# Performance work log

Hardware: AMD Instinct MI355X
Metric: run time of the kernel (lower is better)

## Reference

```python
import jax, jax.numpy as jnp
import numpy as np

N_HEADS = 16


def setup_inputs() -> dict:
    key = jax.random.key(0)
    ks = jax.random.split(key, 5)
    B, S, D = 2, 2048, 1024
    x = jax.random.normal(ks[0], (B, S, D), dtype=jnp.float32)
    Wqkv = jax.random.normal(ks[1], (D, 3 * D), dtype=jnp.float32) * (1.0 / np.sqrt(D))
    bqkv = jax.random.normal(ks[2], (3 * D,), dtype=jnp.float32) * 0.02
    Wout = jax.random.normal(ks[3], (D, D), dtype=jnp.float32) * (1.0 / np.sqrt(D))
    bout = jax.random.normal(ks[4], (D,), dtype=jnp.float32) * 0.02
    return {"x": x, "Wqkv": Wqkv, "bqkv": bqkv, "Wout": Wout, "bout": bout}


def reference(x, Wqkv, bqkv, Wout, bout):
    B, S, D = x.shape
    H = N_HEADS
    dh = D // H
    # qkv projection, then view as [B,S,H,3*dh] and chunk on last dim
    # (matches torch: per-head q/k/v are interleaved slices of the projection)
    qkv = (x @ Wqkv + bqkv).reshape(B, S, H, 3 * dh).transpose(0, 2, 1, 3)  # [B,H,S,3dh]
    q, k, v = jnp.split(qkv, 3, axis=-1)  # each [B,H,S,dh]
    scale = jnp.asarray(1.0 / np.sqrt(dh), dtype=x.dtype)
    scores = jnp.einsum('bhqd,bhkd->bhqk', q, k) * scale  # [B,H,S,S]
    causal = jnp.tril(jnp.ones((S, S), dtype=bool))
    scores = jnp.where(causal, scores, jnp.asarray(-jnp.inf, dtype=scores.dtype))
    attn_w = jax.nn.softmax(scores, axis=-1)
    attn = jnp.einsum('bhqk,bhkd->bhqd', attn_w, v)  # [B,H,S,dh]
    attn = attn.transpose(0, 2, 1, 3).reshape(B, S, D)
    return attn @ Wout + bout
```

## Files before the change

### kernel.cpp

```cpp
#include <hip/hip_runtime.h>
#include <hip/hip_bf16.h>
#include <cstdint>
#include <cstddef>

typedef __hip_bfloat16 bf16;
typedef short bf16x4 __attribute__((ext_vector_type(4)));
typedef short bf16x8 __attribute__((ext_vector_type(8)));
typedef float f32x4 __attribute__((ext_vector_type(4)));

#define LOG2E 1.44269504088896f

static constexpr int Bb = 2, S = 2048, D = 1024, H = 16, DH = 64;

__device__ inline short f2bf_bits(float f) {
  bf16 b = __float2bfloat16(f);
  short s;
  __builtin_memcpy(&s, &b, 2);
  return s;
}
__device__ inline float bfbits2f(short s) {
  uint32_t u = ((uint32_t)(uint16_t)s) << 16;
  float f;
  __builtin_memcpy(&f, &u, 4);
  return f;
}

__global__ void transpose_cvt_k(const float* __restrict__ in, bf16* __restrict__ out,
                                int R, int C) {
  __shared__ float t[32][33];
  int c0 = blockIdx.x * 32, r0 = blockIdx.y * 32;
  int tx = threadIdx.x, ty = threadIdx.y;
#pragma unroll
  for (int i = 0; i < 4; i++) {
    int r = ty + i * 8;
    t[r][tx] = in[(size_t)(r0 + r) * C + c0 + tx];
  }
  __syncthreads();
#pragma unroll
  for (int i = 0; i < 4; i++) {
    int c = ty + i * 8;
    out[(size_t)(c0 + c) * R + r0 + tx] = __float2bfloat16(t[tx][c]);
  }
}

__global__ void cvt_f32_bf16_k(const float* __restrict__ in, bf16* __restrict__ out) {
  size_t i = ((size_t)blockIdx.x * 256 + threadIdx.x) * 8;
  f32x4 a = *(const f32x4*)(in + i);
  f32x4 b = *(const f32x4*)(in + i + 4);
  bf16x8 v;
#pragma unroll
  for (int j = 0; j < 4; j++) { v[j] = f2bf_bits(a[j]); v[4 + j] = f2bf_bits(b[j]); }
  *(bf16x8*)((short*)out + i) = v;
}

__global__ __launch_bounds__(256) void gemm_qkv(
    const bf16* __restrict__ A, const bf16* __restrict__ Bt,
    const float* __restrict__ bias,
    bf16* __restrict__ Qb, bf16* __restrict__ Kb, bf16* __restrict__ Vtb) {
  constexpr int K = 1024;
  __shared__ __align__(16) short smA[128 * 32];
  __shared__ __align__(16) short smB[128 * 32];

  const int tid = threadIdx.x;
  const int wave = tid >> 6, lane = tid & 63;
  const int quad = lane >> 4, l16 = lane & 15;
  const int m0 = blockIdx.y * 128, n0 = blockIdx.x * 128;
  const int wm = wave >> 1, wn = wave & 1;

  f32x4 acc[4][4];
#pragma unroll
  for (int i = 0; i < 4; i++)
#pragma unroll
    for (int j = 0; j < 4; j++) acc[i][j] = {0.f, 0.f, 0.f, 0.f};

  const int srow = lane >> 2;
  const int scol = (lane & 3) * 8;

  for (int k0 = 0; k0 < K; k0 += 32) {
#pragma unroll
    for (int half = 0; half < 2; half++) {
      int row = half * 64 + wave * 16 + srow;
      const bf16* ga = A + (size_t)(m0 + row) * K + k0 + scol;
      const bf16* gb = Bt + (size_t)(n0 + row) * K + k0 + scol;
      __builtin_amdgcn_global_load_lds(
          (const __attribute__((address_space(1))) void*)ga,
          (__attribute__((address_space(3))) void*)&smA[(half * 64 + wave * 16) * 32],
          16, 0, 0);
      __builtin_amdgcn_global_load_lds(
          (const __attribute__((address_space(1))) void*)gb,
          (__attribute__((address_space(3))) void*)&smB[(half * 64 + wave * 16) * 32],
          16, 0, 0);
    }
    __syncthreads();

    bf16x8 af[4], bf_[4];
#pragma unroll
    for (int mi = 0; mi < 4; mi++)
      af[mi] = *(const bf16x8*)&smA[(wm * 64 + mi * 16 + l16) * 32 + quad * 8];
#pragma unroll
    for (int ni = 0; ni < 4; ni++)
      bf_[ni] = *(const bf16x8*)&smB[(wn * 64 + ni * 16 + l16) * 32 + quad * 8];
#pragma unroll
    for (int mi = 0; mi < 4; mi++)
#pragma unroll
      for (int ni = 0; ni < 4; ni++)
        acc[mi][ni] = __builtin_amdgcn_mfma_f32_16x16x32_bf16(
            af[mi], bf_[ni], acc[mi][ni], 0, 0, 0);
    __syncthreads();
  }

#pragma unroll
  for (int ni = 0; ni < 4; ni++) {
    const int cs = n0 + wn * 64 + ni * 16;
    const int h = cs / 192;
    const int roff = cs - h * 192;
    const float bv = bias[cs + l16];
#pragma unroll
    for (int mi = 0; mi < 4; mi++) {
      const int t0 = m0 + wm * 64 + mi * 16 + quad * 4;
      const int b = t0 >> 11, s0 = t0 & 2047;
      if (roff < 64) {
        const int dh = roff + l16;
        size_t base = ((size_t)(b * H + h) * S + s0) * 64 + dh;
#pragma unroll
        for (int r = 0; r < 4; r++)
          Qb[base + (size_t)r * 64] = __float2bfloat16(acc[mi][ni][r] + bv);
      } else if (roff < 128) {
        const int dh = roff - 64 + l16;
        size_t base = ((size_t)(b * H + h) * S + s0) * 64 + dh;
#pragma unroll
        for (int r = 0; r < 4; r++)
          Kb[base + (size_t)r * 64] = __float2bfloat16(acc[mi][ni][r] + bv);
      } else {
        const int dh = roff - 128 + l16;
        size_t base = ((size_t)(b * H + h) * 64 + dh) * S + s0;
        bf16x4 vv;
#pragma unroll
        for (int r = 0; r < 4; r++) vv[r] = f2bf_bits(acc[mi][ni][r] + bv);
        *(bf16x4*)((short*)Vtb + base) = vv;
      }
    }
  }
}

template <typename TC, int BN>
__global__ __launch_bounds__(256) void gemm_bt_bias(
    const bf16* __restrict__ A, const bf16* __restrict__ Bt,
    const float* __restrict__ bias, TC* __restrict__ C,
    int M, int N, int K) {
  constexpr int NF = BN / 32;
  __shared__ __align__(16) short smA[128 * 32];
  __shared__ __align__(16) short smB[BN * 32];

  const int tid = threadIdx.x;
  const int wave = tid >> 6, lane = tid & 63;
  const int quad = lane >> 4, l16 = lane & 15;
  const int m0 = blockIdx.y * 128, n0 = blockIdx.x * BN;
  const int wm = wave >> 1, wn = wave & 1;

  f32x4 acc[4][NF];
#pragma unroll
  for (int i = 0; i < 4; i++)
#pragma unroll
    for (int j = 0; j < NF; j++) acc[i][j] = {0.f, 0.f, 0.f, 0.f};

  const int srow = lane >> 2;
  const int scol = (lane & 3) * 8;

  for (int k0 = 0; k0 < K; k0 += 32) {
#pragma unroll
    for (int half = 0; half < 2; half++) {
      int row = half * 64 + wave * 16 + srow;
      const bf16* ga = A + (size_t)(m0 + row) * K + k0 + scol;
      __builtin_amdgcn_global_load_lds(
          (const __attribute__((address_space(1))) void*)ga,
          (__attribute__((address_space(3))) void*)&smA[(half * 64 + wave * 16) * 32],
          16, 0, 0);
    }
#pragma unroll
    for (int half = 0; half < BN / 64; half++) {
      int row = half * 64 + wave * 16 + srow;
      const bf16* gb = Bt + (size_t)(n0 + row) * K + k0 + scol;
      __builtin_amdgcn_global_load_lds(
          (const __attribute__((address_space(1))) void*)gb,
          (__attribute__((address_space(3))) void*)&smB[(half * 64 + wave * 16) * 32],
          16, 0, 0);
    }
    __syncthreads();

    bf16x8 af[4], bf_[NF];
#pragma unroll
    for (int mi = 0; mi < 4; mi++)
      af[mi] = *(const bf16x8*)&smA[(wm * 64 + mi * 16 + l16) * 32 + quad * 8];
#pragma unroll
    for (int ni = 0; ni < NF; ni++)
      bf_[ni] = *(const bf16x8*)&smB[(wn * (BN / 2) + ni * 16 + l16) * 32 + quad * 8];
#pragma unroll
    for (int mi = 0; mi < 4; mi++)
#pragma unroll
      for (int ni = 0; ni < NF; ni++)
        acc[mi][ni] = __builtin_amdgcn_mfma_f32_16x16x32_bf16(
            af[mi], bf_[ni], acc[mi][ni], 0, 0, 0);
    __syncthreads();
  }

#pragma unroll
  for (int ni = 0; ni < NF; ni++) {
    int col = n0 + wn * (BN / 2) + ni * 16 + l16;
    float bv = bias[col];
#pragma unroll
    for (int mi = 0; mi < 4; mi++) {
#pragma unroll
      for (int r = 0; r < 4; r++) {
        int row = m0 + wm * 64 + mi * 16 + quad * 4 + r;
        float v = acc[mi][ni][r] + bv;
        if constexpr (__is_same(TC, float))
          C[(size_t)row * N + col] = v;
        else
          C[(size_t)row * N + col] = __float2bfloat16(v);
      }
    }
  }
}

__global__ __launch_bounds__(256) void attn_kernel(
    const bf16* __restrict__ Qb, const bf16* __restrict__ Kb,
    const bf16* __restrict__ Vtb,
    bf16* __restrict__ Op0, bf16* __restrict__ Op1,
    float* __restrict__ lp0, float* __restrict__ lp1,
    bf16* __restrict__ Ofinal, int split) {
  const int blk = blockIdx.x;
  int sk, p, bh;
  if (split == 2) { sk = blk & 1; p = (blk >> 1) & 15; bh = blk >> 5; }
  else            { sk = 0;       p = blk & 15;        bh = blk >> 4; }
  const int h = bh & (H - 1), b = bh >> 4;
  const int tid = threadIdx.x;
  const int wave = tid >> 6, lane = tid & 63;
  const int quad = lane >> 4, l16 = lane & 15;

  bf16* __restrict__ Op = sk ? Op1 : Op0;
  float* __restrict__ lp = sk ? lp1 : lp0;

  const bf16* Qh = Qb + (size_t)(b * H + h) * S * 64;
  const bf16* Kh = Kb + (size_t)(b * H + h) * S * 64;
  const bf16* Vth = Vtb + (size_t)(b * H + h) * 64 * S;

  __shared__ __align__(16) short smK[64 * 64];
  __shared__ __align__(16) short smVt[64 * 64];
  __shared__ __align__(16) short pLds[4][16][76];

  const int lrow = lane >> 3;
  const int lg = lane & 7;
  const float PSCALE = 0.125f * LOG2E;
  const int swz = l16 & 7;

#pragma unroll
  for (int pass = 0; pass < 2; pass++) {
    const int qt = pass ? p : (31 - p);
    const int q0 = qt * 64 + wave * 16;

    bf16x8 aQ[2];
#pragma unroll
    for (int kh = 0; kh < 2; kh++)
      aQ[kh] = *(const bf16x8*)(Qh + (size_t)(q0 + l16) * 64 + kh * 32 + quad * 8);

    f32x4 o[4];
#pragma unroll
    for (int dt = 0; dt < 4; dt++) o[dt] = {0.f, 0.f, 0.f, 0.f};
    float lsum[4] = {0.f, 0.f, 0.f, 0.f};

    for (int it = sk; it <= qt; it += split) {
      const int kv0 = it * 64;
      __syncthreads();

#pragma unroll
      for (int j = 0; j < 2; j++) {
        const int row = wave * 16 + j * 8 + lrow;
        const bf16* ks = Kh + (size_t)(kv0 + row) * 64 + (lg ^ (row & 7)) * 8;
        __builtin_amdgcn_global_load_lds(
            (const __attribute__((address_space(1))) void*)ks,
            (__attribute__((address_space(3))) void*)&smK[(wave * 16 + j * 8) * 64],
            16, 0, 0);
        const bf16* vs = Vth + (size_t)row * S + kv0 + (lg ^ (row & 7)) * 8;
        __builtin_amdgcn_global_load_lds(
            (const __attribute__((address_space(1))) void*)vs,
            (__attribute__((address_space(3))) void*)&smVt[(wave * 16 + j * 8) * 64],
            16, 0, 0);
      }
      __syncthreads();

      f32x4 z[4];
#pragma unroll
      for (int nh = 0; nh < 4; nh++) {
        const int row = nh * 16 + l16;
        f32x4 t = {0.f, 0.f, 0.f, 0.f};
#pragma unroll
        for (int kh = 0; kh < 2; kh++) {
          bf16x8 bK = *(const bf16x8*)&smK[row * 64 + ((kh * 4 + quad) ^ swz) * 8];
          t = __builtin_amdgcn_mfma_f32_16x16x32_bf16(aQ[kh], bK, t, 0, 0, 0);
        }
        z[nh] = t;
      }

      const bool full = (it < qt);

#pragma unroll
      for (int r = 0; r < 4; r++) {
        const int qrow = wave * 16 + quad * 4 + r;
        float pv[4];
#pragma unroll
        for (int nh = 0; nh < 4; nh++) {
          float e = exp2f(z[nh][r] * PSCALE);
          pv[nh] = (full || (nh * 16 + l16 <= qrow)) ? e : 0.f;
        }
        lsum[r] += (pv[0] + pv[1]) + (pv[2] + pv[3]);
#pragma unroll
        for (int nh = 0; nh < 4; nh++)
          pLds[wave][quad * 4 + r][nh * 16 + l16] = f2bf_bits(pv[nh]);
      }

      asm volatile("s_waitcnt lgkmcnt(0)" ::: "memory");

      bf16x8 aP[2];
#pragma unroll
      for (int k2 = 0; k2 < 2; k2++)
        aP[k2] = *(const bf16x8*)&pLds[wave][l16][k2 * 32 + quad * 8];
#pragma unroll
      for (int dt = 0; dt < 4; dt++) {
        const int row = dt * 16 + l16;
#pragma unroll
        for (int k2 = 0; k2 < 2; k2++) {
          bf16x8 bV = *(const bf16x8*)&smVt[row * 64 + ((k2 * 4 + quad) ^ swz) * 8];
          o[dt] = __builtin_amdgcn_mfma_f32_16x16x32_bf16(aP[k2], bV, o[dt], 0, 0, 0);
        }
      }
    }

#pragma unroll
    for (int r = 0; r < 4; r++) {
      float l = lsum[r];
#pragma unroll
      for (int d = 1; d < 16; d <<= 1) l += __shfl_xor(l, d, 64);
      const int q = q0 + quad * 4 + r;
      const size_t row = (size_t)(b * H + h) * S + q;
      if (split == 2) {
        if (l16 == 0) lp[row] = l;
#pragma unroll
        for (int dt = 0; dt < 4; dt++)
          ((short*)Op)[row * 64 + dt * 16 + l16] = f2bf_bits(o[dt][r]);
      } else {
        const float inv = 1.f / l;
#pragma unroll
        for (int dt = 0; dt < 4; dt++)
          Ofinal[(size_t)(b * S + q) * D + h * 64 + dt * 16 + l16] =
              __float2bfloat16(o[dt][r] * inv);
      }
    }
  }
}

__global__ __launch_bounds__(256) void attn_reduce(
    const bf16* __restrict__ O0, const bf16* __restrict__ O1,
    const float* __restrict__ l0, const float* __restrict__ l1,
    bf16* __restrict__ attnO) {
  int gid = blockIdx.x * 256 + threadIdx.x;
  int row = gid >> 3;
  int c8 = (gid & 7) * 8;
  float inv = 1.f / (l0[row] + l1[row]);
  bf16x8 a = *(const bf16x8*)((const short*)O0 + (size_t)row * 64 + c8);
  bf16x8 bb = *(const bf16x8*)((const short*)O1 + (size_t)row * 64 + c8);
  bf16x8 o;
#pragma unroll
  for (int j = 0; j < 8; j++)
    o[j] = f2bf_bits((bfbits2f(a[j]) + bfbits2f(bb[j])) * inv);
  int bh = row >> 11, q = row & 2047;
  int b = bh >> 4, h = bh & 15;
  *(bf16x8*)((short*)attnO + (((size_t)(b * S + q) * H + h) * 64 + c8)) = o;
}

extern "C" void kernel_launch(void* const* d_in, const int* in_sizes, int n_in,
                              void* d_out, int out_size, void* d_ws, size_t ws_size,
                              hipStream_t stream) {
  const float* x    = (const float*)d_in[0];
  const float* Wqkv = (const float*)d_in[1];
  const float* bqkv = (const float*)d_in[2];
  const float* Wout = (const float*)d_in[3];
  const float* bout = (const float*)d_in[4];
  float* out = (float*)d_out;

  char* ws = (char*)d_ws;
  const bool split2 = (ws_size >= 50855936);

  bf16* Qb  = (bf16*)(ws);
  bf16* Kb  = (bf16*)(ws + 8388608);
  bf16* Vtb = (bf16*)(ws + 16777216);
  bf16* xbf = (bf16*)(ws + 25165824);

  bf16 *Op0, *Op1, *attnO;
  float *lp0, *lp1;
  bf16 *wqkvT, *woutT;
  if (split2) {
    Op0   = (bf16*)(ws + 25165824);
    Op1   = (bf16*)(ws + 33554432);
    lp0   = (float*)(ws + 41943040);
    lp1   = (float*)(ws + 42205184);
    attnO = (bf16*)(ws + 8388608);
    wqkvT = (bf16*)(ws + 42467328);
    woutT = (bf16*)(ws + 48758784);
  } else {
    Op0 = Op1 = nullptr; lp0 = lp1 = nullptr;
    attnO = (bf16*)(ws + 25165824);
    wqkvT = (bf16*)(ws + 33554432);
    woutT = (bf16*)(ws + 39845888);
  }

  transpose_cvt_k<<<dim3(3072 / 32, 1024 / 32), dim3(32, 8), 0, stream>>>(Wqkv, wqkvT, 1024, 3072);
  transpose_cvt_k<<<dim3(1024 / 32, 1024 / 32), dim3(32, 8), 0, stream>>>(Wout, woutT, 1024, 1024);
  cvt_f32_bf16_k<<<dim3(4096 * 1024 / (256 * 8)), 256, 0, stream>>>(x, xbf);

  gemm_qkv<<<dim3(3072 / 128, 4096 / 128), 256, 0, stream>>>(
      xbf, wqkvT, bqkv, Qb, Kb, Vtb);

  if (split2) {
    attn_kernel<<<dim3(1024), 256, 0, stream>>>(
        Qb, Kb, Vtb, Op0, Op1, lp0, lp1, nullptr, 2);
    attn_reduce<<<dim3(2048), 256, 0, stream>>>(Op0, Op1, lp0, lp1, attnO);
  } else {
    attn_kernel<<<dim3(512), 256, 0, stream>>>(
        Qb, Kb, Vtb, nullptr, nullptr, nullptr, nullptr, attnO, 1);
  }

  gemm_bt_bias<float, 64><<<dim3(1024 / 64, 4096 / 128), 256, 0, stream>>>(
      attnO, woutT, bout, out, 4096, 1024, 1024);
}
```

Before: 197.8 us.

## Fuse prep kernels and stage GEMM epilogues through LDS for vectorized stores

```diff
diff --git a/kernel.cpp b/kernel.cpp
--- a/kernel.cpp
+++ b/kernel.cpp
@@ -25,32 +25,41 @@
   return f;
 }
 
-__global__ void transpose_cvt_k(const float* __restrict__ in, bf16* __restrict__ out,
-                                int R, int C) {
-  __shared__ float t[32][33];
-  int c0 = blockIdx.x * 32, r0 = blockIdx.y * 32;
-  int tx = threadIdx.x, ty = threadIdx.y;
-#pragma unroll
-  for (int i = 0; i < 4; i++) {
-    int r = ty + i * 8;
-    t[r][tx] = in[(size_t)(r0 + r) * C + c0 + tx];
-  }
-  __syncthreads();
-#pragma unroll
-  for (int i = 0; i < 4; i++) {
-    int c = ty + i * 8;
-    out[(size_t)(c0 + c) * R + r0 + tx] = __float2bfloat16(t[tx][c]);
-  }
-}
-
-__global__ void cvt_f32_bf16_k(const float* __restrict__ in, bf16* __restrict__ out) {
-  size_t i = ((size_t)blockIdx.x * 256 + threadIdx.x) * 8;
-  f32x4 a = *(const f32x4*)(in + i);
-  f32x4 b = *(const f32x4*)(in + i + 4);
-  bf16x8 v;
-#pragma unroll
-  for (int j = 0; j < 4; j++) { v[j] = f2bf_bits(a[j]); v[4 + j] = f2bf_bits(b[j]); }
-  *(bf16x8*)((short*)out + i) = v;
+__global__ __launch_bounds__(256) void prep_kernel(
+    const float* __restrict__ Wqkv, bf16* __restrict__ wqkvT,
+    const float* __restrict__ Wout, bf16* __restrict__ woutT,
+    const float* __restrict__ x, bf16* __restrict__ xbf) {
+  const int blk = blockIdx.x;
+  const int tid = threadIdx.x;
+  if (blk < 4096) {
+    __shared__ float t[32][33];
+    const float* in;
+    bf16* out;
+    int R, C, bx, by;
+    if (blk < 3072) { in = Wqkv; out = wqkvT; R = 1024; C = 3072; bx = blk % 96; by = blk / 96; }
+    else            { in = Wout; out = woutT; R = 1024; C = 1024; bx = (blk - 3072) % 32; by = (blk - 3072) / 32; }
+    int c0 = bx * 32, r0 = by * 32;
+    int tx = tid & 31, ty = tid >> 5;
+#pragma unroll
+    for (int i = 0; i < 4; i++) {
+      int r = ty + i * 8;
+      t[r][tx] = in[(size_t)(r0 + r) * C + c0 + tx];
+    }
+    __syncthreads();
+#pragma unroll
+    for (int i = 0; i < 4; i++) {
+      int c = ty + i * 8;
+      out[(size_t)(c0 + c) * R + r0 + tx] = __float2bfloat16(t[tx][c]);
+    }
+  } else {
+    size_t i = ((size_t)(blk - 4096) * 256 + tid) * 8;
+    f32x4 a = *(const f32x4*)(x + i);
+    f32x4 b = *(const f32x4*)(x + i + 4);
+    bf16x8 v;
+#pragma unroll
+    for (int j = 0; j < 4; j++) { v[j] = f2bf_bits(a[j]); v[4 + j] = f2bf_bits(b[j]); }
+    *(bf16x8*)((short*)xbf + i) = v;
+  }
 }
 
 __global__ __launch_bounds__(256) void gemm_qkv(
@@ -60,6 +69,7 @@
   constexpr int K = 1024;
   __shared__ __align__(16) short smA[128 * 32];
   __shared__ __align__(16) short smB[128 * 32];
+  __shared__ __align__(16) short smE[4][16 * 72];
 
   const int tid = threadIdx.x;
   const int wave = tid >> 6, lane = tid & 63;
@@ -109,48 +119,60 @@
     __syncthreads();
   }
 
-#pragma unroll
-  for (int ni = 0; ni < 4; ni++) {
-    const int cs = n0 + wn * 64 + ni * 16;
-    const int h = cs / 192;
-    const int roff = cs - h * 192;
-    const float bv = bias[cs + l16];
+  const int cs0 = n0 + wn * 64;
+  const int h = cs0 / 192;
+  const int rt = (cs0 >> 6) % 3;
+  const int t0w = m0 + wm * 64;
+  const int b = t0w >> 11, s0w = t0w & 2047;
+
+  float bv[4];
+#pragma unroll
+  for (int ni = 0; ni < 4; ni++) bv[ni] = bias[cs0 + ni * 16 + l16];
+
+  if (rt < 2) {
+    bf16* dst = (rt == 0 ? Qb : Kb) + ((size_t)(b * H + h) * S + s0w) * 64;
+    short* sE = &smE[wave][0];
+    const int r8 = lane >> 2, s4 = lane & 3;
 #pragma unroll
     for (int mi = 0; mi < 4; mi++) {
-      const int t0 = m0 + wm * 64 + mi * 16 + quad * 4;
-      const int b = t0 >> 11, s0 = t0 & 2047;
-      if (roff < 64) {
-        const int dh = roff + l16;
-        size_t base = ((size_t)(b * H + h) * S + s0) * 64 + dh;
+#pragma unroll
+      for (int ni = 0; ni < 4; ni++)
 #pragma unroll
         for (int r = 0; r < 4; r++)
-          Qb[base + (size_t)r * 64] = __float2bfloat16(acc[mi][ni][r] + bv);
-      } else if (roff < 128) {
-        const int dh = roff - 64 + l16;
-        size_t base = ((size_t)(b * H + h) * S + s0) * 64 + dh;
-#pragma unroll
-        for (int r = 0; r < 4; r++)
-          Kb[base + (size_t)r * 64] = __float2bfloat16(acc[mi][ni][r] + bv);
-      } else {
-        const int dh = roff - 128 + l16;
+          sE[(quad * 4 + r) * 72 + ni * 16 + l16] = f2bf_bits(acc[mi][ni][r] + bv[ni]);
+      asm volatile("s_waitcnt lgkmcnt(0)" ::: "memory");
+      bf16x8 w0 = *(const bf16x8*)&sE[r8 * 72 + s4 * 16];
+      bf16x8 w1 = *(const bf16x8*)&sE[r8 * 72 + s4 * 16 + 8];
+      short* g = (short*)dst + (size_t)(mi * 16 + r8) * 64 + s4 * 16;
+      *(bf16x8*)g = w0;
+      *(bf16x8*)(g + 8) = w1;
+      asm volatile("s_waitcnt lgkmcnt(0)" ::: "memory");
+    }
+  } else {
+#pragma unroll
+    for (int ni = 0; ni < 4; ni++) {
+      const int dh = ni * 16 + l16;
+#pragma unroll
+      for (int mi = 0; mi < 4; mi++) {
+        const int s0 = s0w + mi * 16 + quad * 4;
         size_t base = ((size_t)(b * H + h) * 64 + dh) * S + s0;
         bf16x4 vv;
 #pragma unroll
-        for (int r = 0; r < 4; r++) vv[r] = f2bf_bits(acc[mi][ni][r] + bv);
+        for (int r = 0; r < 4; r++) vv[r] = f2bf_bits(acc[mi][ni][r] + bv[ni]);
         *(bf16x4*)((short*)Vtb + base) = vv;
       }
     }
   }
 }
 
-template <typename TC, int BN>
-__global__ __launch_bounds__(256) void gemm_bt_bias(
+__global__ __launch_bounds__(256) void gemm_out(
     const bf16* __restrict__ A, const bf16* __restrict__ Bt,
-    const float* __restrict__ bias, TC* __restrict__ C,
+    const float* __restrict__ bias, float* __restrict__ C,
     int M, int N, int K) {
-  constexpr int NF = BN / 32;
+  constexpr int BN = 64, NF = 2;
   __shared__ __align__(16) short smA[128 * 32];
   __shared__ __align__(16) short smB[BN * 32];
+  __shared__ __align__(16) float smEf[4][580];
 
   const int tid = threadIdx.x;
   const int wave = tid >> 6, lane = tid & 63;
@@ -177,13 +199,12 @@
           (__attribute__((address_space(3))) void*)&smA[(half * 64 + wave * 16) * 32],
           16, 0, 0);
     }
-#pragma unroll
-    for (int half = 0; half < BN / 64; half++) {
-      int row = half * 64 + wave * 16 + srow;
+    {
+      int row = wave * 16 + srow;
       const bf16* gb = Bt + (size_t)(n0 + row) * K + k0 + scol;
       __builtin_amdgcn_global_load_lds(
           (const __attribute__((address_space(1))) void*)gb,
-          (__attribute__((address_space(3))) void*)&smB[(half * 64 + wave * 16) * 32],
+          (__attribute__((address_space(3))) void*)&smB[(wave * 16) * 32],
           16, 0, 0);
     }
     __syncthreads();
@@ -194,7 +215,7 @@
       af[mi] = *(const bf16x8*)&smA[(wm * 64 + mi * 16 + l16) * 32 + quad * 8];
 #pragma unroll
     for (int ni = 0; ni < NF; ni++)
-      bf_[ni] = *(const bf16x8*)&smB[(wn * (BN / 2) + ni * 16 + l16) * 32 + quad * 8];
+      bf_[ni] = *(const bf16x8*)&smB[(wn * 32 + ni * 16 + l16) * 32 + quad * 8];
 #pragma unroll
     for (int mi = 0; mi < 4; mi++)
 #pragma unroll
@@ -204,22 +225,29 @@
     __syncthreads();
   }
 
-#pragma unroll
-  for (int ni = 0; ni < NF; ni++) {
-    int col = n0 + wn * (BN / 2) + ni * 16 + l16;
-    float bv = bias[col];
-#pragma unroll
-    for (int mi = 0; mi < 4; mi++) {
-#pragma unroll
-      for (int r = 0; r < 4; r++) {
-        int row = m0 + wm * 64 + mi * 16 + quad * 4 + r;
-        float v = acc[mi][ni][r] + bv;
-        if constexpr (__is_same(TC, float))
-          C[(size_t)row * N + col] = v;
-        else
-          C[(size_t)row * N + col] = __float2bfloat16(v);
-      }
-    }
+  float bv[NF];
+#pragma unroll
+  for (int ni = 0; ni < NF; ni++) bv[ni] = bias[n0 + wn * 32 + ni * 16 + l16];
+
+  float* sE = &smEf[wave][0];
+#pragma unroll
+  for (int mi = 0; mi < 4; mi++) {
+#pragma unroll
+    for (int ni = 0; ni < NF; ni++)
+#pragma unroll
+      for (int r = 0; r < 4; r++)
+        sE[(quad * 4 + r) * 36 + ni * 16 + l16] = acc[mi][ni][r] + bv[ni];
+    asm volatile("s_waitcnt lgkmcnt(0)" ::: "memory");
+#pragma unroll
+    for (int t = 0; t < 2; t++) {
+      int slot = t * 64 + lane;
+      int rr = slot >> 3, c4 = slot & 7;
+      f32x4 v = *(const f32x4*)&sE[rr * 36 + c4 * 4];
+      int row = m0 + wm * 64 + mi * 16 + rr;
+      int col = n0 + wn * 32 + c4 * 4;
+      *(f32x4*)&C[(size_t)row * N + col] = v;
+    }
+    asm volatile("s_waitcnt lgkmcnt(0)" ::: "memory");
   }
 }
 
@@ -414,9 +442,7 @@
     woutT = (bf16*)(ws + 39845888);
   }
 
-  transpose_cvt_k<<<dim3(3072 / 32, 1024 / 32), dim3(32, 8), 0, stream>>>(Wqkv, wqkvT, 1024, 3072);
-  transpose_cvt_k<<<dim3(1024 / 32, 1024 / 32), dim3(32, 8), 0, stream>>>(Wout, woutT, 1024, 1024);
-  cvt_f32_bf16_k<<<dim3(4096 * 1024 / (256 * 8)), 256, 0, stream>>>(x, xbf);
+  prep_kernel<<<dim3(6144), 256, 0, stream>>>(Wqkv, wqkvT, Wout, woutT, x, xbf);
 
   gemm_qkv<<<dim3(3072 / 128, 4096 / 128), 256, 0, stream>>>(
       xbf, wqkvT, bqkv, Qb, Kb, Vtb);
@@ -430,6 +456,6 @@
         Qb, Kb, Vtb, nullptr, nullptr, nullptr, nullptr, attnO, 1);
   }
 
-  gemm_bt_bias<float, 64><<<dim3(1024 / 64, 4096 / 128), 256, 0, stream>>>(
+  gemm_out<<<dim3(1024 / 64, 4096 / 128), 256, 0, stream>>>(
       attnO, woutT, bout, out, 4096, 1024, 1024);
 }
```

After: 193.4 us. -2.2%, faster.
